# Performance work log

Measured on AMD Instinct MI355X. Metric: run time of the kernel, lower is better.

The kernel has to match this reference:

```python
import jax, jax.numpy as jnp
import numpy as np

N, D = 8192, 1024
TEMPERATURE = 0.1
EPS = 1e-8

def setup_inputs() -> dict:
    key = jax.random.key(0)
    k1, k2 = jax.random.split(key)
    emb = jax.random.normal(k1, (N, D), dtype=jnp.float32)
    # docstring: embeddings are normalized
    emb = emb / jnp.linalg.norm(emb, axis=1, keepdims=True)
    labels = jax.random.randint(k2, (N,), 0, 2, dtype=jnp.int32)
    return {"embeddings": emb, "labels": labels}

def reference(embeddings, labels):
    lab = labels.astype(embeddings.dtype)            # (N,)
    sim = jnp.matmul(embeddings, embeddings.T) / TEMPERATURE  # (N, N)
    exp_sim = jnp.exp(sim)                           # original uses raw exp (no max-subtract)
    diag = jnp.diagonal(exp_sim)                     # self-similarity exp(1/T)
    # all_sim excludes self; pos_sim = other reference rows (labels==1, j != i)
    all_sum = exp_sim.sum(axis=1) - diag             # (N,)
    pos_sum = exp_sim @ lab - diag * lab             # subtract self only when i is ref
    loss_per_row = -jnp.log(pos_sum / (all_sum + EPS))
    n_ref = lab.sum()
    loss = jnp.sum(jnp.where(lab > 0, loss_per_row, 0.0)) / jnp.maximum(n_ref, 1.0)
    # original returns 0.0 when fewer than 2 reference rows
    return jnp.where(n_ref < 2, jnp.array(0.0, embeddings.dtype), loss)
```

## Files before the change

kernel.cpp:

```cpp
#include <hip/hip_runtime.h>
#include <hip/hip_bf16.h>
#include <cstdint>
#include <cstddef>

#define NROWS 8192
#define DIM   1024
#define BT    256
#define BK    64
#define NKT   (DIM / BK)
#define NFULL 496
#define NDIAG 32
#define NBLK  (NFULL + NDIAG)
#define EPS 1e-8f
#define PRESCALE 3.798288f

#define ABUF_E 16384
#define BUF_E  32768

typedef short  bf16x8  __attribute__((ext_vector_type(8)));
typedef float  floatx4 __attribute__((ext_vector_type(4)));

typedef __attribute__((address_space(1))) const void CGV;
typedef __attribute__((address_space(3))) void LV;

__device__ __forceinline__ void async_load16(const void* g, void* l) {
    __builtin_amdgcn_global_load_lds((CGV*)g, (LV*)l, 16, 0, 0);
}

__device__ __forceinline__ unsigned short f2bf_rne(float f) {
    union { float f; unsigned u; } c; c.f = f;
    unsigned u = c.u;
    unsigned r = (u + 0x7fffu + ((u >> 16) & 1u)) >> 16;
    return (unsigned short)r;
}

__global__ __launch_bounds__(256) void convert_kernel(
    const float* __restrict__ in, unsigned short* __restrict__ out,
    float* __restrict__ accum )
{
    int i = (blockIdx.x * 256 + threadIdx.x) * 4;
    float4 v = *(const float4*)(in + i);
    ushort4 o;
    o.x = f2bf_rne(v.x * PRESCALE);
    o.y = f2bf_rne(v.y * PRESCALE);
    o.z = f2bf_rne(v.z * PRESCALE);
    o.w = f2bf_rne(v.w * PRESCALE);
    *(ushort4*)(out + i) = o;
    if (blockIdx.x < (2 * NROWS) / 256)
        accum[blockIdx.x * 256 + threadIdx.x] = 0.0f;
}

__global__ __launch_bounds__(512, 2) void gemm_fused_kernel(
    const unsigned short* __restrict__ E,
    const int*            __restrict__ labels,
    float*                __restrict__ all_sum,
    float*                __restrict__ pos_sum)
{
    __shared__ __align__(16) unsigned short S[2 * BUF_E];

    const int tid  = threadIdx.x;
    const int lane = tid & 63;
    const int w    = tid >> 6;
    const int wm   = (w < 4) ? 1 : 0;
    const int wn   = (w < 4) ? w : ((0x0132 >> ((w & 3) * 4)) & 0xF);
    const int colw = lane & 15;
    const int quad = lane >> 4;
    const int swz  = colw & 7;

    const int b = blockIdx.x;
    int rBase, cBase; bool isDiag;
    if (b < NFULL) {
        const int t = (b & 7) * 62 + (b >> 3);
        int a = (int)((1.0f + sqrtf(1.0f + 8.0f * (float)t)) * 0.5f);
        while (a * (a - 1) / 2 > t) --a;
        while ((a + 1) * a / 2 <= t) ++a;
        const int c = t - a * (a - 1) / 2;
        rBase = a * BT; cBase = c * BT; isDiag = false;
    } else {
        const int p = b - NFULL;
        rBase = p * BT; cBase = rBase; isDiag = true;
    }

    const int l8  = lane >> 3;
    const int gch = (lane & 7) ^ l8;
    const unsigned short* gA0 = E + (size_t)(rBase + w * 32 + l8) * DIM + gch * 8;
    const unsigned short* gB0 = E + (size_t)(cBase + w * 32 + l8) * DIM + gch * 8;
    const int aL = w * 2048 + lane * 8;

    floatx4 acc[8][4];
    #pragma unroll
    for (int i = 0; i < 8; ++i)
        #pragma unroll
        for (int j = 0; j < 4; ++j)
            acc[i][j] = (floatx4)0.0f;

#define STAGE(T, SB) do {                                                     \
        const unsigned short* _ga = gA0 + (T) * BK;                           \
        const unsigned short* _gb = gB0 + (T) * BK;                           \
        unsigned short* _la = &S[(SB) * BUF_E + aL];                          \
        unsigned short* _lb = &S[(SB) * BUF_E + ABUF_E + aL];                 \
        _Pragma("unroll")                                                     \
        for (int j = 0; j < 4; ++j) {                                         \
            async_load16(_ga + j * (8 * DIM), _la + j * 512);                 \
            async_load16(_gb + j * (8 * DIM), _lb + j * 512);                 \
        }                                                                     \
    } while (0)

#define KLOOP(MASKCHECK)                                                      \
    for (int kt = 0; kt < NKT; ++kt) {                                        \
        const int bb = (kt & 1) * BUF_E;                                      \
        _Pragma("unroll")                                                     \
        for (int ksub = 0; ksub < 2; ++ksub) {                                \
            const int cs = (((ksub << 2) | quad) ^ swz) << 3;                 \
            bf16x8 bF[4], aF[8];                                              \
            _Pragma("unroll")                                                 \
            for (int nt = 0; nt < 4; ++nt)                                    \
                bF[nt] = *(const bf16x8*)&S[bb + ABUF_E +                     \
                              (wn * 64 + nt * 16 + colw) * BK + cs];          \
            _Pragma("unroll")                                                 \
            for (int mt = 0; mt < 8; ++mt)                                    \
                aF[mt] = *(const bf16x8*)&S[bb +                              \
                              (wm * 128 + mt * 16 + colw) * BK + cs];         \
            __builtin_amdgcn_s_setprio(1);                                    \
            _Pragma("unroll")                                                 \
            for (int mt = 0; mt < 8; ++mt)                                    \
                _Pragma("unroll")                                             \
                for (int nt = 0; nt < 4; ++nt)                                \
                    if (MASKCHECK)                                            \
                        acc[mt][nt] = __builtin_amdgcn_mfma_f32_16x16x32_bf16(\
                            aF[mt], bF[nt], acc[mt][nt], 0, 0, 0);            \
            __builtin_amdgcn_s_setprio(0);                                    \
        }                                                                     \
        __builtin_amdgcn_sched_barrier(0);                                    \
        __builtin_amdgcn_s_barrier();            \
        __builtin_amdgcn_sched_barrier(0);                                    \
        if (kt < NKT - 2) {                                                   \
            STAGE(kt + 2, kt & 1);                                            \
            asm volatile("s_waitcnt vmcnt(8)" ::: "memory");                  \
        } else {                                                              \
            asm volatile("s_waitcnt vmcnt(0)" ::: "memory");                  \
        }                                                                     \
        __builtin_amdgcn_s_barrier();                \
        __builtin_amdgcn_sched_barrier(0);                                    \
    }

    STAGE(0, 0);
    STAGE(1, 1);
    asm volatile("s_waitcnt vmcnt(8)" ::: "memory");
    __builtin_amdgcn_s_barrier();
    __builtin_amdgcn_sched_barrier(0);

    if (!isDiag) {
        KLOOP(true)
    } else {
        KLOOP(wm * 128 + mt * 16 + 15 >= wn * 64 + nt * 16)
    }
#undef KLOOP
#undef STAGE

    float labc[4];
    int   gcolv[4];
    #pragma unroll
    for (int nt = 0; nt < 4; ++nt) {
        gcolv[nt] = cBase + wn * 64 + nt * 16 + colw;
        labc[nt]  = (float)labels[gcolv[nt]];
    }

    float colAll[4] = {0.f, 0.f, 0.f, 0.f};
    float colPos[4] = {0.f, 0.f, 0.f, 0.f};

    #pragma unroll
    for (int mt = 0; mt < 8; ++mt) {
        const int growBase = rBase + wm * 128 + mt * 16 + quad * 4;
        #pragma unroll
        for (int r = 0; r < 4; ++r) {
            const int grow = growBase + r;
            const float labr = (float)labels[grow];
            float sAll = 0.f, sPos = 0.f;
            #pragma unroll
            for (int nt = 0; nt < 4; ++nt) {
                float ev = exp2f(acc[mt][nt][r]);
                ev = (grow > gcolv[nt]) ? ev : 0.0f;
                sAll += ev;
                sPos += ev * labc[nt];
                colAll[nt] += ev;
                colPos[nt] += ev * labr;
            }
            #pragma unroll
            for (int off = 1; off < 16; off <<= 1) {
                sAll += __shfl_xor(sAll, off);
                sPos += __shfl_xor(sPos, off);
            }
            if (colw == 0 && sAll != 0.f) {
                atomicAdd(&all_sum[grow], sAll);
                atomicAdd(&pos_sum[grow], sPos);
            }
        }
    }

    #pragma unroll
    for (int nt = 0; nt < 4; ++nt) {
        float aa = colAll[nt], p = colPos[nt];
        aa += __shfl_xor(aa, 16);  p += __shfl_xor(p, 16);
        aa += __shfl_xor(aa, 32);  p += __shfl_xor(p, 32);
        if (quad == 0 && aa != 0.f) {
            atomicAdd(&all_sum[gcolv[nt]], aa);
            atomicAdd(&pos_sum[gcolv[nt]], p);
        }
    }
}

__global__ __launch_bounds__(1024) void finalize_kernel(
    const float* __restrict__ all_sum,
    const float* __restrict__ pos_sum,
    const int*   __restrict__ labels,
    float*       __restrict__ out)
{
    __shared__ float sSum[1024];
    __shared__ float sCnt[1024];
    const int tid = threadIdx.x;
    float lsum = 0.f, lcnt = 0.f;
    for (int i = tid; i < NROWS; i += 1024) {
        if (labels[i] > 0) {
            float p = pos_sum[i];
            float a = all_sum[i] + EPS;
            lsum += -logf(p / a);
            lcnt += 1.0f;
        }
    }
    sSum[tid] = lsum;
    sCnt[tid] = lcnt;
    __syncthreads();
    for (int s = 512; s > 0; s >>= 1) {
        if (tid < s) { sSum[tid] += sSum[tid + s]; sCnt[tid] += sCnt[tid + s]; }
        __syncthreads();
    }
    if (tid == 0) {
        float n = sCnt[0];
        out[0] = (n < 2.0f) ? 0.0f : sSum[0] / fmaxf(n, 1.0f);
    }
}

extern "C" void kernel_launch(void* const* d_in, const int* in_sizes, int n_in,
                              void* d_out, int out_size, void* d_ws, size_t ws_size,
                              hipStream_t stream) {
    const float* emb    = (const float*)d_in[0];
    const int*   labels = (const int*)d_in[1];
    float*       out    = (float*)d_out;

    unsigned short* Ebf = (unsigned short*)d_ws;
    const size_t embBytes = (size_t)NROWS * DIM * sizeof(unsigned short);
    float* all_sum = (float*)((char*)d_ws + embBytes);
    float* pos_sum = all_sum + NROWS;

    convert_kernel<<<(NROWS * DIM) / (4 * 256), 256, 0, stream>>>(emb, Ebf, all_sum);

    gemm_fused_kernel<<<NBLK, 512, 0, stream>>>(Ebf, labels, all_sum, pos_sum);

    finalize_kernel<<<1, 1024, 0, stream>>>(all_sum, pos_sum, labels, out);
}
```

Measured before the change: 226.5 us.

## Interleave staged loads with split-phase MFMA compute and pair diagonal tiles per block

Restructures the GEMM main loop into four phases per k-tile, issuing the next tiles' async global-to-LDS loads in pieces between MFMA phases so that memory traffic overlaps with compute at finer grain. Diagonal tiles skip loading the B operand because A and B are the same rows, and their masking becomes a compile-time template path. Each diagonal block now processes two diagonal tiles in sequence, halving the number of diagonal blocks so the grid has fewer, more even blocks. The costs are extra barriers per k-tile, a changed wave-to-subtile mapping, and diagonal blocks that each take longer to finish.

```diff
diff --git a/kernel.cpp b/kernel.cpp
--- a/kernel.cpp
+++ b/kernel.cpp
@@ -9,8 +9,8 @@
 #define BK    64
 #define NKT   (DIM / BK)
 #define NFULL 496
-#define NDIAG 32
-#define NBLK  (NFULL + NDIAG)
+#define NDD   16
+#define NBLK  (NFULL + NDD)
 #define EPS 1e-8f
 #define PRESCALE 3.798288f
 
@@ -50,42 +50,46 @@
         accum[blockIdx.x * 256 + threadIdx.x] = 0.0f;
 }
 
-__global__ __launch_bounds__(512, 2) void gemm_fused_kernel(
+template<bool DIAG>
+__device__ __forceinline__ void run_tile(
     const unsigned short* __restrict__ E,
     const int*            __restrict__ labels,
     float*                __restrict__ all_sum,
-    float*                __restrict__ pos_sum)
+    float*                __restrict__ pos_sum,
+    unsigned short* S, int rBase, int cBase)
 {
-    __shared__ __align__(16) unsigned short S[2 * BUF_E];
-
     const int tid  = threadIdx.x;
     const int lane = tid & 63;
     const int w    = tid >> 6;
-    const int wm   = (w < 4) ? 1 : 0;
-    const int wn   = (w < 4) ? w : ((0x0132 >> ((w & 3) * 4)) & 0xF);
+    const int wm   = w >> 2;
+    const int wn   = (w < 4) ? w : ((0x1023 >> ((w & 3) * 4)) & 0xF);
     const int colw = lane & 15;
     const int quad = lane >> 4;
     const int swz  = colw & 7;
-
-    const int b = blockIdx.x;
-    int rBase, cBase; bool isDiag;
-    if (b < NFULL) {
-        const int t = (b & 7) * 62 + (b >> 3);
-        int a = (int)((1.0f + sqrtf(1.0f + 8.0f * (float)t)) * 0.5f);
-        while (a * (a - 1) / 2 > t) --a;
-        while ((a + 1) * a / 2 <= t) ++a;
-        const int c = t - a * (a - 1) / 2;
-        rBase = a * BT; cBase = c * BT; isDiag = false;
-    } else {
-        const int p = b - NFULL;
-        rBase = p * BT; cBase = rBase; isDiag = true;
-    }
+    const int cs0  = ((0 | quad) ^ swz) << 3;
+    const int cs1  = ((4 | quad) ^ swz) << 3;
 
     const int l8  = lane >> 3;
     const int gch = (lane & 7) ^ l8;
-    const unsigned short* gA0 = E + (size_t)(rBase + w * 32 + l8) * DIM + gch * 8;
-    const unsigned short* gB0 = E + (size_t)(cBase + w * 32 + l8) * DIM + gch * 8;
-    const int aL = w * 2048 + lane * 8;
+    const unsigned short* gA = E + (size_t)(rBase + w * 8 + l8) * DIM + gch * 8;
+    const unsigned short* gB = E + (size_t)(cBase + w * 8 + l8) * DIM + gch * 8;
+    const int ldsT = w * 512 + lane * 8;
+
+#define STG_A(rb, T, dB) async_load16(gA + (size_t)(rb) * DIM + (T) * BK,   \
+                                      &S[(dB) + (rb) * 64 + ldsT])
+#define STG_B(rb, T, dB) async_load16(gB + (size_t)(rb) * DIM + (T) * BK,   \
+                                      &S[(dB) + ABUF_E + (rb) * 64 + ldsT])
+
+    unsigned liveMask = 0xFFFFFFFFu;
+    if (DIAG) {
+        liveMask = 0u;
+        #pragma unroll
+        for (int mt = 0; mt < 8; ++mt)
+            #pragma unroll
+            for (int nt = 0; nt < 4; ++nt)
+                if (wm * 128 + mt * 16 + 15 >= wn * 64 + nt * 16)
+                    liveMask |= 1u << (mt * 4 + nt);
+    }
 
     floatx4 acc[8][4];
     #pragma unroll
@@ -94,69 +98,84 @@
         for (int j = 0; j < 4; ++j)
             acc[i][j] = (floatx4)0.0f;
 
-#define STAGE(T, SB) do {                                                     \
-        const unsigned short* _ga = gA0 + (T) * BK;                           \
-        const unsigned short* _gb = gB0 + (T) * BK;                           \
-        unsigned short* _la = &S[(SB) * BUF_E + aL];                          \
-        unsigned short* _lb = &S[(SB) * BUF_E + ABUF_E + aL];                 \
-        _Pragma("unroll")                                                     \
-        for (int j = 0; j < 4; ++j) {                                         \
-            async_load16(_ga + j * (8 * DIM), _la + j * 512);                 \
-            async_load16(_gb + j * (8 * DIM), _lb + j * 512);                 \
-        }                                                                     \
-    } while (0)
-
-#define KLOOP(MASKCHECK)                                                      \
-    for (int kt = 0; kt < NKT; ++kt) {                                        \
-        const int bb = (kt & 1) * BUF_E;                                      \
-        _Pragma("unroll")                                                     \
-        for (int ksub = 0; ksub < 2; ++ksub) {                                \
-            const int cs = (((ksub << 2) | quad) ^ swz) << 3;                 \
-            bf16x8 bF[4], aF[8];                                              \
-            _Pragma("unroll")                                                 \
-            for (int nt = 0; nt < 4; ++nt)                                    \
-                bF[nt] = *(const bf16x8*)&S[bb + ABUF_E +                     \
-                              (wn * 64 + nt * 16 + colw) * BK + cs];          \
-            _Pragma("unroll")                                                 \
-            for (int mt = 0; mt < 8; ++mt)                                    \
-                aF[mt] = *(const bf16x8*)&S[bb +                              \
-                              (wm * 128 + mt * 16 + colw) * BK + cs];         \
-            __builtin_amdgcn_s_setprio(1);                                    \
-            _Pragma("unroll")                                                 \
-            for (int mt = 0; mt < 8; ++mt)                                    \
-                _Pragma("unroll")                                             \
-                for (int nt = 0; nt < 4; ++nt)                                \
-                    if (MASKCHECK)                                            \
-                        acc[mt][nt] = __builtin_amdgcn_mfma_f32_16x16x32_bf16(\
-                            aF[mt], bF[nt], acc[mt][nt], 0, 0, 0);            \
-            __builtin_amdgcn_s_setprio(0);                                    \
-        }                                                                     \
-        __builtin_amdgcn_sched_barrier(0);                                    \
-        __builtin_amdgcn_s_barrier();            \
-        __builtin_amdgcn_sched_barrier(0);                                    \
-        if (kt < NKT - 2) {                                                   \
-            STAGE(kt + 2, kt & 1);                                            \
-            asm volatile("s_waitcnt vmcnt(8)" ::: "memory");                  \
-        } else {                                                              \
-            asm volatile("s_waitcnt vmcnt(0)" ::: "memory");                  \
-        }                                                                     \
-        __builtin_amdgcn_s_barrier();                \
-        __builtin_amdgcn_sched_barrier(0);                                    \
-    }
-
-    STAGE(0, 0);
-    STAGE(1, 1);
-    asm volatile("s_waitcnt vmcnt(8)" ::: "memory");
+    STG_A(0, 0, 0);  STG_A(128, 0, 0);
+    STG_A(64, 0, 0); STG_A(192, 0, 0);
+    if (!DIAG) { STG_B(0, 0, 0); STG_B(64, 0, 0);
+                 STG_B(128, 0, 0); STG_B(192, 0, 0); }
+    STG_A(0, 1, BUF_E); STG_A(128, 1, BUF_E);
+    asm volatile("s_waitcnt vmcnt(2)" ::: "memory");
     __builtin_amdgcn_s_barrier();
     __builtin_amdgcn_sched_barrier(0);
 
-    if (!isDiag) {
-        KLOOP(true)
-    } else {
-        KLOOP(wm * 128 + mt * 16 + 15 >= wn * 64 + nt * 16)
-    }
-#undef KLOOP
-#undef STAGE
+    bf16x8 bFr[2][4];
+
+#define PH_READB(KS, CS)                                                      \
+    _Pragma("unroll")                                                         \
+    for (int nt = 0; nt < 4; ++nt)                                            \
+        bFr[KS][nt] = *(const bf16x8*)&S[bRegion +                            \
+                          (wn * 64 + nt * 16 + colw) * BK + (CS)];
+
+#define PH_COMPUTE(M, KS, CS)                                                 \
+    {                                                                         \
+        bf16x8 aF[4];                                                         \
+        _Pragma("unroll")                                                     \
+        for (int i = 0; i < 4; ++i)                                           \
+            aF[i] = *(const bf16x8*)&S[bb +                                   \
+                        (wm * 128 + ((M) * 4 + i) * 16 + colw) * BK + (CS)];  \
+        __builtin_amdgcn_s_setprio(1);                                        \
+        _Pragma("unroll")                                                     \
+        for (int i = 0; i < 4; ++i) {                                         \
+            _Pragma("unroll")                                                 \
+            for (int nt = 0; nt < 4; ++nt) {                                  \
+                if (!DIAG || ((liveMask >> ((((M) * 4 + i) * 4) + nt)) & 1u)) \
+                    acc[(M) * 4 + i][nt] =                                    \
+                        __builtin_amdgcn_mfma_f32_16x16x32_bf16(              \
+                            aF[i], bFr[KS][nt], acc[(M) * 4 + i][nt], 0, 0, 0);\
+            }                                                                 \
+        }                                                                     \
+        __builtin_amdgcn_s_setprio(0);                                        \
+    }
+
+#define BARSEQ  __builtin_amdgcn_sched_barrier(0);                            \
+                __builtin_amdgcn_s_barrier();                                 \
+                __builtin_amdgcn_sched_barrier(0);
+
+    for (int kt = 0; kt < NKT; ++kt) {
+        const int bb = (kt & 1) ? BUF_E : 0;
+        const int nb = bb ^ BUF_E;
+        const int bRegion = DIAG ? bb : (bb + ABUF_E);
+        const bool s1 = (kt <= NKT - 2);
+        const bool s2 = (kt <= NKT - 3);
+
+        if (s1) {
+            STG_A(64, kt + 1, nb); STG_A(192, kt + 1, nb);
+            if (!DIAG) { STG_B(0, kt + 1, nb); STG_B(64, kt + 1, nb); }
+        }
+        PH_READB(0, cs0)
+        PH_COMPUTE(0, 0, cs0)
+        BARSEQ
+
+        if (s1 && !DIAG) { STG_B(128, kt + 1, nb); STG_B(192, kt + 1, nb); }
+        PH_READB(1, cs1)
+        PH_COMPUTE(0, 1, cs1)
+        BARSEQ
+
+        if (s2) { STG_A(0, kt + 2, bb); STG_A(128, kt + 2, bb); }
+        PH_COMPUTE(1, 0, cs0)
+        BARSEQ
+
+        PH_COMPUTE(1, 1, cs1)
+        __builtin_amdgcn_sched_barrier(0);
+        if (s2) asm volatile("s_waitcnt vmcnt(2)" ::: "memory");
+        else    asm volatile("s_waitcnt vmcnt(0)" ::: "memory");
+        __builtin_amdgcn_s_barrier();
+        __builtin_amdgcn_sched_barrier(0);
+    }
+#undef PH_COMPUTE
+#undef PH_READB
+#undef BARSEQ
+#undef STG_A
+#undef STG_B
 
     float labc[4];
     int   gcolv[4];
@@ -210,6 +229,31 @@
     }
 }
 
+__global__ __launch_bounds__(512, 2) void gemm_fused_kernel(
+    const unsigned short* __restrict__ E,
+    const int*            __restrict__ labels,
+    float*                __restrict__ all_sum,
+    float*                __restrict__ pos_sum)
+{
+    __shared__ __align__(16) unsigned short S[2 * BUF_E];
+
+    const int b = blockIdx.x;
+    if (b < NFULL) {
+        const int t = (b & 7) * 62 + (b >> 3);
+        int a = (int)((1.0f + sqrtf(1.0f + 8.0f * (float)t)) * 0.5f);
+        while (a * (a - 1) / 2 > t) --a;
+        while ((a + 1) * a / 2 <= t) ++a;
+        const int c = t - a * (a - 1) / 2;
+        run_tile<false>(E, labels, all_sum, pos_sum, S, a * BT, c * BT);
+    } else {
+        const int i = b - NFULL;
+        for (int r = 0; r < 2; ++r) {
+            const int d = (2 * i + r) * BT;
+            run_tile<true>(E, labels, all_sum, pos_sum, S, d, d);
+        }
+    }
+}
+
 __global__ __launch_bounds__(1024) void finalize_kernel(
     const float* __restrict__ all_sum,
     const float* __restrict__ pos_sum,
```

Measured after the change: 226.6 us. About the same (+0.0%).
